# Performance work log

Measured on AMD Instinct MI355X. Metric: run time of the kernel, lower is better.

The kernel has to match this reference:

```python
import jax, jax.numpy as jnp
import numpy as np
import math

N_HEAD = 16
N_KV_HEAD = 4
WINDOW = 512
EPS = 1e-6


def _rotate_half(t):
    t1, t2 = jnp.split(t, 2, axis=-1)
    return jnp.concatenate([-t2, t1], axis=-1)


def _rope_tables(T, head_dim):
    theta = 1.0 / (10000.0 ** (jnp.arange(0, head_dim, 2, dtype=jnp.float32) / head_dim))
    pos = jnp.arange(T, dtype=jnp.float32)
    freqs = jnp.outer(pos, theta)                      # [T, d/2]
    cos = jnp.concatenate([jnp.cos(freqs), jnp.cos(freqs)], axis=-1)  # [T, d]
    sin = jnp.concatenate([jnp.sin(freqs), jnp.sin(freqs)], axis=-1)
    return cos, sin


def setup_inputs() -> dict:
    key = jax.random.key(0)
    k1, k2, k3, k4 = jax.random.split(key, 4)
    B, T, C = 1, 2048, 1024
    kv_out = 2 * N_KV_HEAD * (C // N_HEAD)  # 512
    x = jax.random.normal(k1, (B, T, C), dtype=jnp.float32)
    Wq = jax.random.normal(k2, (C, C), dtype=jnp.float32) * 0.02
    Wkv = jax.random.normal(k3, (kv_out, C), dtype=jnp.float32) * 0.02
    Wproj = jax.random.normal(k4, (C, C), dtype=jnp.float32) * 0.02
    return {"x": x, "Wq": Wq, "Wkv": Wkv, "Wproj": Wproj}


def reference(x, Wq, Wkv, Wproj):
    B, T, C = x.shape
    H, KV = N_HEAD, N_KV_HEAD
    d = C // H
    n_rep = H // KV

    q = (x @ Wq.T).reshape(B, T, H, d).transpose(0, 2, 1, 3)     # [B,H,T,d]
    kv = x @ Wkv.T                                               # [B,T,2*KV*d]
    k, v = jnp.split(kv, 2, axis=2)
    k = k.reshape(B, T, KV, d).transpose(0, 2, 1, 3)             # [B,KV,T,d]
    v = v.reshape(B, T, KV, d).transpose(0, 2, 1, 3)

    # QK L2 normalization
    q = q / (jnp.linalg.norm(q, axis=-1, keepdims=True) + EPS)
    k = k / (jnp.linalg.norm(k, axis=-1, keepdims=True) + EPS)

    # RoPE
    cos, sin = _rope_tables(T, d)
    cos = cos[None, None]  # [1,1,T,d]
    sin = sin[None, None]
    q = q * cos + _rotate_half(q) * sin
    k = k * cos + _rotate_half(k) * sin

    # GQA: repeat KV heads (repeat_interleave on head dim)
    k = jnp.repeat(k, n_rep, axis=1)   # [B,H,T,d]
    v = jnp.repeat(v, n_rep, axis=1)

    # sliding-window causal mask: cols <= rows and cols > rows - WINDOW
    rows = jnp.arange(T)[:, None]
    cols = jnp.arange(T)[None, :]
    mask = (cols <= rows) & (cols > rows - WINDOW)  # [T,T] bool

    scale = 1.0 / math.sqrt(d)
    scores = jnp.einsum("bhqd,bhkd->bhqk", q, k) * scale
    scores = jnp.where(mask[None, None], scores, -jnp.inf)
    attn = jax.nn.softmax(scores, axis=-1)
    y = jnp.einsum("bhqk,bhkd->bhqd", attn, v)      # [B,H,T,d]
    y = y.transpose(0, 2, 1, 3).reshape(B, T, C)
    return y @ Wproj.T
```

## Files before the change

kernel.cpp:

```cpp
#include <hip/hip_runtime.h>

#define T_SEQ 2048
#define C_DIM 1024
#define NH    16
#define NKV   4
#define HD    64
#define WIN   512

typedef __bf16 bf16x8 __attribute__((ext_vector_type(8)));
typedef __bf16 bf16x4 __attribute__((ext_vector_type(4)));
typedef float f32x4 __attribute__((ext_vector_type(4)));

#define MFMA16(a, b, c) __builtin_amdgcn_mfma_f32_16x16x32_bf16(a, b, c, 0, 0, 0)

#define GLD16(g, s)                                                          \
  __builtin_amdgcn_global_load_lds(                                          \
      (const __attribute__((address_space(1))) void*)(g),                    \
      (__attribute__((address_space(3))) void*)(s), 16, 0, 0)

__global__ __launch_bounds__(256) void prep_kernel(const float* __restrict__ x,
                                                   const float* __restrict__ Wq,
                                                   const float* __restrict__ Wkv,
                                                   const float* __restrict__ Wp,
                                                   __bf16* __restrict__ xb,
                                                   __bf16* __restrict__ Wqkvb,
                                                   __bf16* __restrict__ Wpb,
                                                   float2* __restrict__ ropeT) {
  int b = blockIdx.x;
  if (b >= 4608) {
    int idx = (b - 4608) * 256 + threadIdx.x;
    int t = idx >> 5, i = idx & 31;
    float theta = exp2f(-(float)i * (13.287712379549449f / 32.0f));
    float s, c;
    sincosf((float)t * theta, &s, &c);
    ropeT[idx] = make_float2(c, s);
    return;
  }
  const float* src;
  __bf16* dst;
  int off;
  if (b < 2048)      { src = x;   dst = xb;                off = b; }
  else if (b < 3072) { src = Wq;  dst = Wqkvb;             off = b - 2048; }
  else if (b < 3584) { src = Wkv; dst = Wqkvb + (1 << 20); off = b - 3072; }
  else               { src = Wp;  dst = Wpb;               off = b - 3584; }
  int i = off * 1024 + threadIdx.x * 4;
  float4 v = *(const float4*)(src + i);
  bf16x4 o;
  o[0] = (__bf16)v.x; o[1] = (__bf16)v.y; o[2] = (__bf16)v.z; o[3] = (__bf16)v.w;
  *(bf16x4*)(dst + i) = o;
}

__device__ __forceinline__ void gemm_core64(const __bf16* __restrict__ A,
                                            const __bf16* __restrict__ B,
                                            int K,
                                            __bf16* AsB, __bf16* BsB,
                                            f32x4 (&acc)[4]) {
  const int tid = threadIdx.x;
  const int w = tid >> 6, l = tid & 63;
  const int quad = l >> 4, r16 = l & 15;
  const int srow = w * 16 + (l >> 3);
  const size_t soff = (size_t)srow * K + (size_t)(((l & 7) ^ (l >> 3)) * 8);
  const __bf16* gA = A + soff;
  const __bf16* gB = B + soff;
  __bf16* const lA = AsB + w * 1024;
  __bf16* const lB = BsB + w * 1024;
  const size_t rstep = (size_t)8 * K;
  int rA[2], rB[4][2];
#pragma unroll
  for (int ks = 0; ks < 2; ++ks) {
    int row = w * 16 + r16;
    rA[ks] = row * 64 + (((ks * 4 + quad) ^ (row & 7)) * 8);
  }
#pragma unroll
  for (int nt = 0; nt < 4; ++nt)
#pragma unroll
    for (int ks = 0; ks < 2; ++ks) {
      int row = nt * 16 + r16;
      rB[nt][ks] = row * 64 + (((ks * 4 + quad) ^ (row & 7)) * 8);
    }
  const int nIter = K >> 6;
  GLD16(gA, lA);
  GLD16(gA + rstep, lA + 512);
  GLD16(gB, lB);
  GLD16(gB + rstep, lB + 512);
  __syncthreads();
  int cur = 0;
  for (int it = 0; it < nIter; ++it) {
    if (it + 1 < nIter) {
      const __bf16* ga = gA + ((it + 1) << 6);
      const __bf16* gb = gB + ((it + 1) << 6);
      __bf16* la = lA + ((cur ^ 1) << 12);
      __bf16* lb = lB + ((cur ^ 1) << 12);
      GLD16(ga, la);
      GLD16(ga + rstep, la + 512);
      GLD16(gb, lb);
      GLD16(gb + rstep, lb + 512);
    }
    const __bf16* Asc = AsB + (cur << 12);
    const __bf16* Bsc = BsB + (cur << 12);
#pragma unroll
    for (int ks = 0; ks < 2; ++ks) {
      bf16x8 fa  = *(const bf16x8*)(Asc + rA[ks]);
      bf16x8 fb0 = *(const bf16x8*)(Bsc + rB[0][ks]);
      bf16x8 fb1 = *(const bf16x8*)(Bsc + rB[1][ks]);
      bf16x8 fb2 = *(const bf16x8*)(Bsc + rB[2][ks]);
      bf16x8 fb3 = *(const bf16x8*)(Bsc + rB[3][ks]);
      acc[0] = MFMA16(fa, fb0, acc[0]);
      acc[1] = MFMA16(fa, fb1, acc[1]);
      acc[2] = MFMA16(fa, fb2, acc[2]);
      acc[3] = MFMA16(fa, fb3, acc[3]);
    }
    if (it + 1 < nIter) {
      __syncthreads();
      cur ^= 1;
    }
  }
}

__global__ __launch_bounds__(256) void gemm_qkv_kernel(const __bf16* __restrict__ xb,
                                                       const __bf16* __restrict__ Wqkvb,
                                                       const float2* __restrict__ ropeT,
                                                       __bf16* __restrict__ Qb,
                                                       __bf16* __restrict__ Kb,
                                                       __bf16* __restrict__ Vt) {
  __shared__ __align__(16) __bf16 smem[16384];
  __bf16* AsB = smem;
  __bf16* BsB = smem + 8192;
  f32x4 acc[4] = {};
  const int m0 = blockIdx.y * 64, n0 = blockIdx.x * 64;
  gemm_core64(xb + (size_t)m0 * C_DIM, Wqkvb + (size_t)n0 * C_DIM, C_DIM, AsB, BsB, acc);
  const int tid = threadIdx.x;
  const int w = tid >> 6, l = tid & 63, quad = l >> 4, r16 = l & 15;
  if (n0 < 1280) {
    const bool isQ = n0 < 1024;
    const int head = isQ ? (n0 >> 6) : ((n0 - 1024) >> 6);
    __bf16* dstBase = (isQ ? Qb : Kb) + (size_t)head * T_SEQ * HD;
    const float osc = isQ ? 0.125f : 1.0f;
#pragma unroll
    for (int r = 0; r < 4; ++r) {
      float ss = acc[0][r] * acc[0][r] + acc[1][r] * acc[1][r] +
                 acc[2][r] * acc[2][r] + acc[3][r] * acc[3][r];
#pragma unroll
      for (int m = 1; m < 16; m <<= 1) ss += __shfl_xor(ss, m, 64);
      const float inv = osc / (sqrtf(ss) + 1e-6f);
      const int t = m0 + w * 16 + quad * 4 + r;
      const float2 cs0 = ropeT[t * 32 + r16];
      const float2 cs1 = ropeT[t * 32 + 16 + r16];
      const float v0 = acc[0][r] * inv, v1 = acc[1][r] * inv;
      const float v2 = acc[2][r] * inv, v3 = acc[3][r] * inv;
      __bf16* dst = dstBase + (size_t)t * HD;
      dst[r16]      = (__bf16)(v0 * cs0.x - v2 * cs0.y);
      dst[16 + r16] = (__bf16)(v1 * cs1.x - v3 * cs1.y);
      dst[32 + r16] = (__bf16)(v2 * cs0.x + v0 * cs0.y);
      dst[48 + r16] = (__bf16)(v3 * cs1.x + v1 * cs1.y);
    }
  } else {
    const int kvh = (n0 - 1280) >> 6;
    __syncthreads();
    __bf16* Vs = smem;
#pragma unroll
    for (int nt = 0; nt < 4; ++nt)
#pragma unroll
      for (int r = 0; r < 4; ++r)
        Vs[(nt * 16 + r16) * 136 + w * 16 + quad * 4 + r] = (__bf16)acc[nt][r];
    __syncthreads();
    const int d = tid >> 2, tc = (tid & 3) * 16;
    __bf16* dst = Vt + ((size_t)kvh * HD + d) * T_SEQ + m0 + tc;
    bf16x8 v0 = *(const bf16x8*)(Vs + d * 136 + tc);
    bf16x8 v1 = *(const bf16x8*)(Vs + d * 136 + tc + 8);
    *(bf16x8*)dst = v0;
    *(bf16x8*)(dst + 8) = v1;
  }
}

__global__ __launch_bounds__(256) void gemm_proj_kernel(const __bf16* __restrict__ Yb,
                                                        const __bf16* __restrict__ Wpb,
                                                        float* __restrict__ C) {
  __shared__ __align__(16) __bf16 smem[16384];
  __bf16* AsB = smem;
  __bf16* BsB = smem + 8192;
  f32x4 acc[4] = {};
  const int m0 = blockIdx.y * 64, n0 = blockIdx.x * 64;
  gemm_core64(Yb + (size_t)m0 * C_DIM, Wpb + (size_t)n0 * C_DIM, C_DIM, AsB, BsB, acc);
  const int tid = threadIdx.x;
  const int w = tid >> 6, l = tid & 63, quad = l >> 4, r16 = l & 15;
  const int mrow = m0 + w * 16 + quad * 4;
  const int ncol = n0 + r16;
#pragma unroll
  for (int r = 0; r < 4; ++r) {
    size_t rowoff = (size_t)(mrow + r) * C_DIM;
    C[rowoff + ncol]      = acc[0][r];
    C[rowoff + ncol + 16] = acc[1][r];
    C[rowoff + ncol + 32] = acc[2][r];
    C[rowoff + ncol + 48] = acc[3][r];
  }
}

__global__ __launch_bounds__(256) void attn_mfma_kernel(const __bf16* __restrict__ Qb,
                                                        const __bf16* __restrict__ Kb,
                                                        const __bf16* __restrict__ Vt,
                                                        __bf16* __restrict__ Yb) {
  __shared__ __align__(16) __bf16 Pl[4][16][72];
  __shared__ __align__(16) float Oc[2][16][68];
  __shared__ float Ls[2][16];
  const int h = blockIdx.y, kvh = h >> 2;
  const int t0 = blockIdx.x * 32;
  const int tid = threadIdx.x;
  const int w = tid >> 6, l = tid & 63;
  const int quad = l >> 4, r16 = l & 15;
  const int sub = w & 1, half = w >> 1;
  const __bf16* qptr = Qb + ((size_t)h * T_SEQ + t0 + sub * 16 + r16) * HD + quad * 8;
  bf16x8 aq0 = *(const bf16x8*)(qptr);
  bf16x8 aq1 = *(const bf16x8*)(qptr + 32);
  const int keyStart = max(0, t0 - (WIN - 1)) & ~63;
  const int keyEnd = (t0 + 32 + 63) & ~63;
  const int nch = (keyEnd - keyStart) >> 6;
  const int nch2 = (nch + 1) >> 1;
  const int cbeg = half ? nch2 : 0;
  const int cend = half ? nch : nch2;
  const __bf16* kbase = Kb + (size_t)kvh * T_SEQ * HD;
  const __bf16* vbase = Vt + (size_t)kvh * HD * T_SEQ;
  const int tq_base = t0 + sub * 16 + quad * 4;
  f32x4 oacc[4] = {};
  float lsum[4] = {0.f, 0.f, 0.f, 0.f};
  for (int c = cbeg; c < cend; ++c) {
    const int key0 = keyStart + (c << 6);
    f32x4 s[4] = {};
#pragma unroll
    for (int nt = 0; nt < 4; ++nt) {
      const __bf16* kr = kbase + (size_t)(key0 + nt * 16 + r16) * HD + quad * 8;
      bf16x8 bk0 = *(const bf16x8*)kr;
      bf16x8 bk1 = *(const bf16x8*)(kr + 32);
      s[nt] = MFMA16(aq0, bk0, s[nt]);
      s[nt] = MFMA16(aq1, bk1, s[nt]);
    }
#pragma unroll
    for (int nt = 0; nt < 4; ++nt) {
      const int key = key0 + nt * 16 + r16;
#pragma unroll
      for (int r = 0; r < 4; ++r) {
        const int tq = tq_base + r;
        bool valid = (key <= tq) && (key > tq - WIN);
        float p = valid ? __expf(s[nt][r]) : 0.0f;
        lsum[r] += p;
        Pl[w][quad * 4 + r][nt * 16 + r16] = (__bf16)p;
      }
    }
    bf16x8 ap0 = *(const bf16x8*)(&Pl[w][r16][quad * 8]);
    bf16x8 ap1 = *(const bf16x8*)(&Pl[w][r16][32 + quad * 8]);
#pragma unroll
    for (int nt = 0; nt < 4; ++nt) {
      const __bf16* vr = vbase + (size_t)(nt * 16 + r16) * T_SEQ + key0 + quad * 8;
      bf16x8 bv0 = *(const bf16x8*)vr;
      bf16x8 bv1 = *(const bf16x8*)(vr + 32);
      oacc[nt] = MFMA16(ap0, bv0, oacc[nt]);
      oacc[nt] = MFMA16(ap1, bv1, oacc[nt]);
    }
  }
#pragma unroll
  for (int r = 0; r < 4; ++r) {
#pragma unroll
    for (int m = 1; m < 16; m <<= 1) lsum[r] += __shfl_xor(lsum[r], m, 64);
  }
  if (half == 1) {
#pragma unroll
    for (int nt = 0; nt < 4; ++nt)
#pragma unroll
      for (int r = 0; r < 4; ++r)
        Oc[sub][quad * 4 + r][nt * 16 + r16] = oacc[nt][r];
    if (r16 == 0) {
#pragma unroll
      for (int r = 0; r < 4; ++r) Ls[sub][quad * 4 + r] = lsum[r];
    }
  }
  __syncthreads();
  if (half == 0) {
#pragma unroll
    for (int r = 0; r < 4; ++r) {
      const float inv = 1.0f / (lsum[r] + Ls[sub][quad * 4 + r]);
      const size_t row = (size_t)(tq_base + r);
#pragma unroll
      for (int nt = 0; nt < 4; ++nt) {
        float o = oacc[nt][r] + Oc[sub][quad * 4 + r][nt * 16 + r16];
        Yb[row * C_DIM + h * HD + nt * 16 + r16] = (__bf16)(o * inv);
      }
    }
  }
}

extern "C" void kernel_launch(void* const* d_in, const int* in_sizes, int n_in,
                              void* d_out, int out_size, void* d_ws, size_t ws_size,
                              hipStream_t stream) {
  const float* x     = (const float*)d_in[0];
  const float* Wq    = (const float*)d_in[1];
  const float* Wkv   = (const float*)d_in[2];
  const float* Wproj = (const float*)d_in[3];
  float* out = (float*)d_out;

  __bf16* xb    = (__bf16*)d_ws;
  __bf16* Wqkvb = xb + (size_t)T_SEQ * C_DIM;
  __bf16* Wpb   = Wqkvb + (size_t)1536 * C_DIM;
  __bf16* Qb    = Wpb + (size_t)C_DIM * C_DIM;
  __bf16* Kb    = Qb + (size_t)NH * T_SEQ * HD;
  __bf16* Vt    = Kb + (size_t)NKV * T_SEQ * HD;
  __bf16* Yb    = Vt + (size_t)NKV * HD * T_SEQ;
  float2* ropeT = (float2*)(Yb + (size_t)T_SEQ * C_DIM);

  prep_kernel<<<4864, 256, 0, stream>>>(x, Wq, Wkv, Wproj, xb, Wqkvb, Wpb, ropeT);
  gemm_qkv_kernel<<<dim3(24, 32), 256, 0, stream>>>(xb, Wqkvb, ropeT, Qb, Kb, Vt);
  attn_mfma_kernel<<<dim3(T_SEQ / 32, NH), 256, 0, stream>>>(Qb, Kb, Vt, Yb);
  gemm_proj_kernel<<<dim3(16, 32), 256, 0, stream>>>(Yb, Wpb, out);
}
```

Measured before the change: 127.6 us.

## Triple-buffer GEMM LDS staging with partial vmcnt waits

Changes the shared GEMM core from double to triple buffering: it prefetches two K-tiles ahead via global_load_lds and waits only for the oldest tile's loads (vmcnt(4)) before a raw s_barrier, instead of a full __syncthreads drain. This is meant to hide global load latency behind the MFMA work. In exchange LDS per block grows from 32KB to 48KB, which may reduce occupancy. The hand-written waitcnt logic depends on the compiler not issuing other vector memory ops in between.

```diff
diff --git a/kernel.cpp b/kernel.cpp
--- a/kernel.cpp
+++ b/kernel.cpp
@@ -17,6 +17,9 @@
   __builtin_amdgcn_global_load_lds(                                          \
       (const __attribute__((address_space(1))) void*)(g),                    \
       (__attribute__((address_space(3))) void*)(s), 16, 0, 0)
+
+#define WAITVM4() asm volatile("s_waitcnt vmcnt(4)" ::: "memory")
+#define WAITVM0() asm volatile("s_waitcnt vmcnt(0)" ::: "memory")
 
 __global__ __launch_bounds__(256) void prep_kernel(const float* __restrict__ x,
                                                    const float* __restrict__ Wq,
@@ -53,7 +56,7 @@
 __device__ __forceinline__ void gemm_core64(const __bf16* __restrict__ A,
                                             const __bf16* __restrict__ B,
                                             int K,
-                                            __bf16* AsB, __bf16* BsB,
+                                            __bf16* smemBase,
                                             f32x4 (&acc)[4]) {
   const int tid = threadIdx.x;
   const int w = tid >> 6, l = tid & 63;
@@ -62,9 +65,8 @@
   const size_t soff = (size_t)srow * K + (size_t)(((l & 7) ^ (l >> 3)) * 8);
   const __bf16* gA = A + soff;
   const __bf16* gB = B + soff;
-  __bf16* const lA = AsB + w * 1024;
-  __bf16* const lB = BsB + w * 1024;
   const size_t rstep = (size_t)8 * K;
+  const int lw = w * 1024;
   int rA[2], rB[4][2];
 #pragma unroll
   for (int ks = 0; ks < 2; ++ks) {
@@ -79,25 +81,33 @@
       rB[nt][ks] = row * 64 + (((ks * 4 + quad) ^ (row & 7)) * 8);
     }
   const int nIter = K >> 6;
-  GLD16(gA, lA);
-  GLD16(gA + rstep, lA + 512);
-  GLD16(gB, lB);
-  GLD16(gB + rstep, lB + 512);
-  __syncthreads();
+
+  auto STAGE = [&](int t, int bi) {
+    __bf16* la = smemBase + bi * 8192 + lw;
+    __bf16* lb = la + 4096;
+    const __bf16* ga = gA + ((size_t)t << 6);
+    const __bf16* gb = gB + ((size_t)t << 6);
+    GLD16(ga, la);
+    GLD16(ga + rstep, la + 512);
+    GLD16(gb, lb);
+    GLD16(gb + rstep, lb + 512);
+  };
+
+  STAGE(0, 0);
+  STAGE(1, 1);
+  WAITVM4();
+  __builtin_amdgcn_s_barrier();
+  __builtin_amdgcn_sched_barrier(0);
+
   int cur = 0;
   for (int it = 0; it < nIter; ++it) {
-    if (it + 1 < nIter) {
-      const __bf16* ga = gA + ((it + 1) << 6);
-      const __bf16* gb = gB + ((it + 1) << 6);
-      __bf16* la = lA + ((cur ^ 1) << 12);
-      __bf16* lb = lB + ((cur ^ 1) << 12);
-      GLD16(ga, la);
-      GLD16(ga + rstep, la + 512);
-      GLD16(gb, lb);
-      GLD16(gb + rstep, lb + 512);
-    }
-    const __bf16* Asc = AsB + (cur << 12);
-    const __bf16* Bsc = BsB + (cur << 12);
+    if (it + 2 < nIter) {
+      int b2 = cur + 2;
+      if (b2 >= 3) b2 -= 3;
+      STAGE(it + 2, b2);
+    }
+    const __bf16* Asc = smemBase + cur * 8192;
+    const __bf16* Bsc = Asc + 4096;
 #pragma unroll
     for (int ks = 0; ks < 2; ++ks) {
       bf16x8 fa  = *(const bf16x8*)(Asc + rA[ks]);
@@ -111,8 +121,14 @@
       acc[3] = MFMA16(fa, fb3, acc[3]);
     }
     if (it + 1 < nIter) {
-      __syncthreads();
-      cur ^= 1;
+      if (it + 2 < nIter) {
+        WAITVM4();
+      } else {
+        WAITVM0();
+      }
+      __builtin_amdgcn_s_barrier();
+      __builtin_amdgcn_sched_barrier(0);
+      cur = (cur == 2) ? 0 : cur + 1;
     }
   }
 }
@@ -123,12 +139,10 @@
                                                        __bf16* __restrict__ Qb,
                                                        __bf16* __restrict__ Kb,
                                                        __bf16* __restrict__ Vt) {
-  __shared__ __align__(16) __bf16 smem[16384];
-  __bf16* AsB = smem;
-  __bf16* BsB = smem + 8192;
+  __shared__ __align__(16) __bf16 smem[24576];
   f32x4 acc[4] = {};
   const int m0 = blockIdx.y * 64, n0 = blockIdx.x * 64;
-  gemm_core64(xb + (size_t)m0 * C_DIM, Wqkvb + (size_t)n0 * C_DIM, C_DIM, AsB, BsB, acc);
+  gemm_core64(xb + (size_t)m0 * C_DIM, Wqkvb + (size_t)n0 * C_DIM, C_DIM, smem, acc);
   const int tid = threadIdx.x;
   const int w = tid >> 6, l = tid & 63, quad = l >> 4, r16 = l & 15;
   if (n0 < 1280) {
@@ -176,12 +190,10 @@
 __global__ __launch_bounds__(256) void gemm_proj_kernel(const __bf16* __restrict__ Yb,
                                                         const __bf16* __restrict__ Wpb,
                                                         float* __restrict__ C) {
-  __shared__ __align__(16) __bf16 smem[16384];
-  __bf16* AsB = smem;
-  __bf16* BsB = smem + 8192;
+  __shared__ __align__(16) __bf16 smem[24576];
   f32x4 acc[4] = {};
   const int m0 = blockIdx.y * 64, n0 = blockIdx.x * 64;
-  gemm_core64(Yb + (size_t)m0 * C_DIM, Wpb + (size_t)n0 * C_DIM, C_DIM, AsB, BsB, acc);
+  gemm_core64(Yb + (size_t)m0 * C_DIM, Wpb + (size_t)n0 * C_DIM, C_DIM, smem, acc);
   const int tid = threadIdx.x;
   const int w = tid >> 6, l = tid & 63, quad = l >> 4, r16 = l & 15;
   const int mrow = m0 + w * 16 + quad * 4;
```

New measurement: 128.3 us. No clear change (+0.5%).

## Stage K/V tiles in LDS with double buffering and 64-query blocks

Applied to the files above, without the earlier changes.

The attention kernel now handles 64 queries per block, one 16-row tile per wave, instead of 32 queries with the key range split between wave halves. Each 64-key chunk of K and V is loaded cooperatively into XOR-swizzled shared memory with async global-to-LDS loads, double-buffered so the next chunk is fetched while the current one is computed. This removes redundant per-wave global K/V reads and the cross-half partial-sum reduction. In exchange it halves the grid size, which lowers parallelism, and adds a block barrier per chunk.

```diff
diff --git a/kernel.cpp b/kernel.cpp
--- a/kernel.cpp
+++ b/kernel.cpp
@@ -200,37 +200,55 @@
                                                         const __bf16* __restrict__ Kb,
                                                         const __bf16* __restrict__ Vt,
                                                         __bf16* __restrict__ Yb) {
+  __shared__ __align__(16) __bf16 KVs[2][8192];
   __shared__ __align__(16) __bf16 Pl[4][16][72];
-  __shared__ __align__(16) float Oc[2][16][68];
-  __shared__ float Ls[2][16];
   const int h = blockIdx.y, kvh = h >> 2;
-  const int t0 = blockIdx.x * 32;
+  const int t0 = blockIdx.x * 64;
   const int tid = threadIdx.x;
   const int w = tid >> 6, l = tid & 63;
   const int quad = l >> 4, r16 = l & 15;
-  const int sub = w & 1, half = w >> 1;
-  const __bf16* qptr = Qb + ((size_t)h * T_SEQ + t0 + sub * 16 + r16) * HD + quad * 8;
+  const int rr = l >> 3;
+  const int cc = (l & 7) ^ rr;
+  const __bf16* qptr = Qb + ((size_t)h * T_SEQ + t0 + w * 16 + r16) * HD + quad * 8;
   bf16x8 aq0 = *(const bf16x8*)(qptr);
   bf16x8 aq1 = *(const bf16x8*)(qptr + 32);
   const int keyStart = max(0, t0 - (WIN - 1)) & ~63;
-  const int keyEnd = (t0 + 32 + 63) & ~63;
-  const int nch = (keyEnd - keyStart) >> 6;
-  const int nch2 = (nch + 1) >> 1;
-  const int cbeg = half ? nch2 : 0;
-  const int cend = half ? nch : nch2;
+  const int nch = ((t0 + 64) - keyStart) >> 6;
   const __bf16* kbase = Kb + (size_t)kvh * T_SEQ * HD;
   const __bf16* vbase = Vt + (size_t)kvh * HD * T_SEQ;
-  const int tq_base = t0 + sub * 16 + quad * 4;
+  const int tq = t0 + w * 16 + quad * 4;
   f32x4 oacc[4] = {};
   float lsum[4] = {0.f, 0.f, 0.f, 0.f};
-  for (int c = cbeg; c < cend; ++c) {
-    const int key0 = keyStart + (c << 6);
+
+  {
+    __bf16* kd = &KVs[0][w * 1024];
+    __bf16* vd = &KVs[0][4096 + w * 1024];
+    const __bf16* kg = kbase + (size_t)(keyStart + w * 16 + rr) * HD + cc * 8;
+    const __bf16* vg = vbase + (size_t)(w * 16 + rr) * T_SEQ + keyStart + cc * 8;
+    GLD16(kg, kd); GLD16(kg + 8 * HD, kd + 512);
+    GLD16(vg, vd); GLD16(vg + 8 * T_SEQ, vd + 512);
+  }
+  __syncthreads();
+  int buf = 0;
+  for (int it = 0; it < nch; ++it) {
+    const int key0 = keyStart + (it << 6);
+    if (it + 1 < nch) {
+      const int kn = key0 + 64;
+      __bf16* kd = &KVs[buf ^ 1][w * 1024];
+      __bf16* vd = &KVs[buf ^ 1][4096 + w * 1024];
+      const __bf16* kg = kbase + (size_t)(kn + w * 16 + rr) * HD + cc * 8;
+      const __bf16* vg = vbase + (size_t)(w * 16 + rr) * T_SEQ + kn + cc * 8;
+      GLD16(kg, kd); GLD16(kg + 8 * HD, kd + 512);
+      GLD16(vg, vd); GLD16(vg + 8 * T_SEQ, vd + 512);
+    }
+    const __bf16* Ksc = &KVs[buf][0];
+    const __bf16* Vsc = &KVs[buf][4096];
     f32x4 s[4] = {};
 #pragma unroll
     for (int nt = 0; nt < 4; ++nt) {
-      const __bf16* kr = kbase + (size_t)(key0 + nt * 16 + r16) * HD + quad * 8;
-      bf16x8 bk0 = *(const bf16x8*)kr;
-      bf16x8 bk1 = *(const bf16x8*)(kr + 32);
+      const int row = nt * 16 + r16;
+      bf16x8 bk0 = *(const bf16x8*)(Ksc + row * 64 + ((quad ^ (row & 7)) * 8));
+      bf16x8 bk1 = *(const bf16x8*)(Ksc + row * 64 + (((4 + quad) ^ (row & 7)) * 8));
       s[nt] = MFMA16(aq0, bk0, s[nt]);
       s[nt] = MFMA16(aq1, bk1, s[nt]);
     }
@@ -239,8 +257,7 @@
       const int key = key0 + nt * 16 + r16;
 #pragma unroll
       for (int r = 0; r < 4; ++r) {
-        const int tq = tq_base + r;
-        bool valid = (key <= tq) && (key > tq - WIN);
+        bool valid = (key <= tq + r) && (key > tq + r - WIN);
         float p = valid ? __expf(s[nt][r]) : 0.0f;
         lsum[r] += p;
         Pl[w][quad * 4 + r][nt * 16 + r16] = (__bf16)p;
@@ -250,41 +267,27 @@
     bf16x8 ap1 = *(const bf16x8*)(&Pl[w][r16][32 + quad * 8]);
 #pragma unroll
     for (int nt = 0; nt < 4; ++nt) {
-      const __bf16* vr = vbase + (size_t)(nt * 16 + r16) * T_SEQ + key0 + quad * 8;
-      bf16x8 bv0 = *(const bf16x8*)vr;
-      bf16x8 bv1 = *(const bf16x8*)(vr + 32);
+      const int d = nt * 16 + r16;
+      bf16x8 bv0 = *(const bf16x8*)(Vsc + d * 64 + ((quad ^ (d & 7)) * 8));
+      bf16x8 bv1 = *(const bf16x8*)(Vsc + d * 64 + (((4 + quad) ^ (d & 7)) * 8));
       oacc[nt] = MFMA16(ap0, bv0, oacc[nt]);
       oacc[nt] = MFMA16(ap1, bv1, oacc[nt]);
     }
+    __syncthreads();
+    buf ^= 1;
   }
 #pragma unroll
   for (int r = 0; r < 4; ++r) {
 #pragma unroll
     for (int m = 1; m < 16; m <<= 1) lsum[r] += __shfl_xor(lsum[r], m, 64);
   }
-  if (half == 1) {
+#pragma unroll
+  for (int r = 0; r < 4; ++r) {
+    const float inv = 1.0f / lsum[r];
+    const size_t row = (size_t)(tq + r);
 #pragma unroll
     for (int nt = 0; nt < 4; ++nt)
-#pragma unroll
-      for (int r = 0; r < 4; ++r)
-        Oc[sub][quad * 4 + r][nt * 16 + r16] = oacc[nt][r];
-    if (r16 == 0) {
-#pragma unroll
-      for (int r = 0; r < 4; ++r) Ls[sub][quad * 4 + r] = lsum[r];
-    }
-  }
-  __syncthreads();
-  if (half == 0) {
-#pragma unroll
-    for (int r = 0; r < 4; ++r) {
-      const float inv = 1.0f / (lsum[r] + Ls[sub][quad * 4 + r]);
-      const size_t row = (size_t)(tq_base + r);
-#pragma unroll
-      for (int nt = 0; nt < 4; ++nt) {
-        float o = oacc[nt][r] + Oc[sub][quad * 4 + r][nt * 16 + r16];
-        Yb[row * C_DIM + h * HD + nt * 16 + r16] = (__bf16)(o * inv);
-      }
-    }
+      Yb[row * C_DIM + h * HD + nt * 16 + r16] = (__bf16)(oacc[nt][r] * inv);
   }
 }
 
@@ -308,6 +311,6 @@
 
   prep_kernel<<<4864, 256, 0, stream>>>(x, Wq, Wkv, Wproj, xb, Wqkvb, Wpb, ropeT);
   gemm_qkv_kernel<<<dim3(24, 32), 256, 0, stream>>>(xb, Wqkvb, ropeT, Qb, Kb, Vt);
-  attn_mfma_kernel<<<dim3(T_SEQ / 32, NH), 256, 0, stream>>>(Qb, Kb, Vt, Yb);
+  attn_mfma_kernel<<<dim3(T_SEQ / 64, NH), 256, 0, stream>>>(Qb, Kb, Vt, Yb);
   gemm_proj_kernel<<<dim3(16, 32), 256, 0, stream>>>(Yb, Wpb, out);
 }
```

New measurement: 107.3 us (median of 2 runs). 15.9% less time.
